# Performance work log

Hardware: AMD Instinct MI355X
Metric: run time of the kernel (lower is better)

The kernel has to match this reference:

```python
import jax, jax.numpy as jnp
import numpy as np
import math

B, LQ, LK = 4, 2048, 2048
DQ = DK = DV = ND = 512
H = 8
DS = ND // H
EPS = 1e-5


def _ln(x, g, b):
    m = jnp.mean(x, axis=-1, keepdims=True)
    v = jnp.mean((x - m) ** 2, axis=-1, keepdims=True)
    return (x - m) / jnp.sqrt(v + EPS) * g + b


def setup_inputs() -> dict:
    key = jax.random.key(0)
    ks = jax.random.split(key, 12)
    s = 0.02
    return {
        "Q": jax.random.normal(ks[0], (B, LQ, DQ), dtype=jnp.float32),
        "K": jax.random.normal(ks[1], (B, LK, DK), dtype=jnp.float32),
        "mask": jax.random.randint(ks[2], (B, LQ, LK), 0, 2, dtype=jnp.int32),
        "temperature": jax.random.uniform(ks[3], (B, LK, 1), dtype=jnp.float32, minval=0.5, maxval=1.5),
        "Wq": jax.random.normal(ks[4], (DQ, ND), dtype=jnp.float32) * s,
        "bq": jnp.zeros((ND,), dtype=jnp.float32),
        "Wk": jax.random.normal(ks[5], (DK, ND), dtype=jnp.float32) * s,
        "bk": jnp.zeros((ND,), dtype=jnp.float32),
        "Wv": jax.random.normal(ks[6], (DK, ND), dtype=jnp.float32) * s,
        "bv": jnp.zeros((ND,), dtype=jnp.float32),
        "Wo": jax.random.normal(ks[7], (ND, ND), dtype=jnp.float32) * s,
        "bo": jnp.zeros((ND,), dtype=jnp.float32),
        "ln0_g": jnp.ones((ND,), dtype=jnp.float32),
        "ln0_b": jnp.zeros((ND,), dtype=jnp.float32),
        "ln1_g": jnp.ones((ND,), dtype=jnp.float32),
        "ln1_b": jnp.zeros((ND,), dtype=jnp.float32),
    }


def reference(Q, K, mask, temperature, Wq, bq, Wk, bk, Wv, bv, Wo, bo, ln0_g, ln0_b, ln1_g, ln1_b):
    q = Q @ Wq + bq                                  # (B, Lq, ND)
    k = K @ Wk + bk                                  # (B, Lk, ND)
    v = K @ Wv + bv                                  # (B, Lk, ND)
    # torch's cat(split(ds,2),0) == head-major reshape; head h -> channels [h*ds:(h+1)*ds]
    qh = q.reshape(B, LQ, H, DS)
    kh = k.reshape(B, LK, H, DS)
    vh = v.reshape(B, LK, H, DS)
    A = jnp.einsum("bqhd,bkhd->bhqk", qh, kh) / math.sqrt(ND)
    # per-key temperature, broadcast over heads and queries
    A = A / temperature[:, None, :, 0][:, :, None, :]      # (B,H,Lq,Lk)
    A = jnp.where(mask[:, None, :, :] == 0, jnp.float32(-1e9), A)
    A = jax.nn.softmax(A, axis=-1)
    Oh = qh + jnp.einsum("bhqk,bkhd->bqhd", A, vh)          # residual with projected Q
    O = Oh.reshape(B, LQ, ND)
    O = _ln(O, ln0_g, ln0_b)
    O = O + jax.nn.relu(O @ Wo + bo)
    O = _ln(O, ln1_g, ln1_b)
    return O
```

## Files before the change

kernel.cpp:

```cpp
#include <hip/hip_runtime.h>

typedef __attribute__((ext_vector_type(8))) short bf16x8;
typedef __attribute__((ext_vector_type(16))) float f32x16;

#define MFMA32 __builtin_amdgcn_mfma_f32_32x32x16_bf16

__device__ __forceinline__ unsigned short bf16r(float f){
  unsigned u = __builtin_bit_cast(unsigned, f);
  unsigned r = (u + 0x7FFFu + ((u >> 16) & 1u)) >> 16;
  return (unsigned short)r;
}
__device__ __forceinline__ unsigned bfpack2(float a, float b){
  unsigned ua = __builtin_bit_cast(unsigned, a);
  unsigned ub = __builtin_bit_cast(unsigned, b);
  unsigned ra = (ua + 0x7FFFu + ((ua >> 16) & 1u)) >> 16;
  unsigned rb = (ub + 0x7FFFu + ((ub >> 16) & 1u)) & 0xFFFF0000u;
  return (ra & 0xFFFFu) | rb;
}
__device__ __forceinline__ float bf2f(unsigned short h){
  unsigned u = ((unsigned)h) << 16;
  return __builtin_bit_cast(float, u);
}
__device__ __forceinline__ unsigned cvtpk_bf16(float a, float b){
  unsigned r;
  asm("v_cvt_pk_bf16_f32 %0, %1, %2" : "=v"(r) : "v"(a), "v"(b));
  return r;
}
__device__ __forceinline__ void permswap(unsigned &x, unsigned &y){
  asm volatile("v_permlane32_swap_b32 %0, %1" : "+v"(x), "+v"(y));
}
__device__ __forceinline__ float fexp2(float x){
  float r; asm("v_exp_f32 %0, %1" : "=v"(r) : "v"(x)); return r;
}

__global__ __launch_bounds__(256) void wt_kernel(
    const float* __restrict__ W0, const float* __restrict__ W1,
    const float* __restrict__ W2, const float* __restrict__ W3,
    unsigned short* __restrict__ T0, unsigned short* __restrict__ T1,
    unsigned short* __restrict__ T2, unsigned short* __restrict__ T3)
{
  int z = blockIdx.z;
  const float* W = z==0?W0 : z==1?W1 : z==2?W2 : W3;
  unsigned short* T = z==0?T0 : z==1?T1 : z==2?T2 : T3;
  __shared__ float tile[64][68];
  int kb0 = blockIdx.x*64, nb0 = blockIdx.y*64;
  int tid = threadIdx.x;
#pragma unroll
  for (int i=0;i<4;++i){
    int c = tid + i*256; int r = c>>4, cc = (c&15)*4;
    *(float4*)&tile[r][cc] = *(const float4*)&W[(kb0+r)*512 + nb0 + cc];
  }
  __syncthreads();
#pragma unroll
  for (int i=0;i<4;++i){
    int c = tid + i*256; int o = c*4; int n = o>>6, kk = o&63;
    ushort4 pk;
    pk.x = bf16r(tile[kk+0][n]); pk.y = bf16r(tile[kk+1][n]);
    pk.z = bf16r(tile[kk+2][n]); pk.w = bf16r(tile[kk+3][n]);
    *(ushort4*)&T[(nb0+n)*512 + kb0 + kk] = pk;
  }
}

__global__ __launch_bounds__(256,2) void qkv_kernel(
    const float* __restrict__ Qin, const float* __restrict__ Kin,
    const unsigned short* __restrict__ WqT, const unsigned short* __restrict__ WkT,
    const unsigned short* __restrict__ WvT,
    const float* __restrict__ bq, const float* __restrict__ bk,
    const float* __restrict__ bv, const float* __restrict__ temp,
    unsigned short* __restrict__ qbuf, unsigned short* __restrict__ kbuf,
    unsigned short* __restrict__ vt)
{
  const float RS2K = 0.044194173824159216f * 1.4426950408889634f;
  __shared__ short SM[128*144];
  short (*As)[72] = (short(*)[72])SM;
  short (*Bs)[72] = (short(*)[72])(SM + 128*72);
  int z = blockIdx.z;
  const float* A = (z==0) ? Qin : Kin;
  const unsigned short* BT = z==0 ? WqT : (z==1 ? WkT : WvT);
  const float* bias = z==0 ? bq : (z==1 ? bk : bv);
  int m0 = blockIdx.x*128, n0 = blockIdx.y*128;
  int tid = threadIdx.x;
  int lane = tid & 63, w = tid >> 6, l5 = lane & 31, hi = lane >> 5;
  int wr = w >> 1, wc = w & 1;
  f32x16 acc00, acc01, acc10, acc11;
#pragma unroll
  for (int i=0;i<16;++i){ acc00[i]=0.f; acc01[i]=0.f; acc10[i]=0.f; acc11[i]=0.f; }

  for (int kt=0; kt<8; ++kt){
    int k0 = kt*64;
    __syncthreads();
#pragma unroll
    for (int i=0;i<4;++i){
      int c = tid + i*256; int r = c>>3, cc = (c&7)*8;
      const float* src = &A[(m0+r)*512 + k0 + cc];
      float4 v0 = *(const float4*)src;
      float4 v1 = *(const float4*)(src+4);
      uint4 pk;
      pk.x = bfpack2(v0.x, v0.y); pk.y = bfpack2(v0.z, v0.w);
      pk.z = bfpack2(v1.x, v1.y); pk.w = bfpack2(v1.z, v1.w);
      *(uint4*)&As[r][cc] = pk;
    }
#pragma unroll
    for (int i=0;i<4;++i){
      int c = tid + i*256; int r = c>>3, cc = (c&7)*8;
      *(uint4*)&Bs[r][cc] = *(const uint4*)&BT[(n0+r)*512 + k0 + cc];
    }
    __syncthreads();
#pragma unroll
    for (int ks=0; ks<4; ++ks){
      bf16x8 a0 = *(const bf16x8*)&As[wr*64 + l5     ][ks*16 + hi*8];
      bf16x8 a1 = *(const bf16x8*)&As[wr*64 + 32 + l5][ks*16 + hi*8];
      bf16x8 b0 = *(const bf16x8*)&Bs[wc*64 + l5     ][ks*16 + hi*8];
      bf16x8 b1 = *(const bf16x8*)&Bs[wc*64 + 32 + l5][ks*16 + hi*8];
      acc00 = MFMA32(a0, b0, acc00, 0,0,0);
      acc01 = MFMA32(a0, b1, acc01, 0,0,0);
      acc10 = MFMA32(a1, b0, acc10, 0,0,0);
      acc11 = MFMA32(a1, b1, acc11, 0,0,0);
    }
  }

  if (z <= 1){
    unsigned short* Cout = (z==0) ? qbuf : kbuf;
#pragma unroll
    for (int mt=0; mt<2; ++mt){
      float sc[16];
      if (z==1){
        int mb = m0 + wr*64 + mt*32 + 4*hi;
#pragma unroll
        for (int qd=0; qd<4; ++qd)
#pragma unroll
        for (int j=0; j<4; ++j)
          sc[qd*4+j] = RS2K*__builtin_amdgcn_rcpf(temp[mb + qd*8 + j]);
      }
#pragma unroll
      for (int nt=0; nt<2; ++nt){
        const f32x16& acc = mt==0 ? (nt==0?acc00:acc01) : (nt==0?acc10:acc11);
        int n = n0 + wc*64 + nt*32 + l5;
        float bn = bias[n];
#pragma unroll
        for (int r=0;r<16;++r){
          int m = m0 + wr*64 + mt*32 + (r&3) + 8*(r>>2) + 4*hi;
          float v = acc[r] + bn;
          if (z==1) v *= sc[r];
          Cout[m*512 + n] = bf16r(v);
        }
      }
    }
  } else {
    __syncthreads();
    short* Lt = SM;
#pragma unroll
    for (int mt=0; mt<2; ++mt)
#pragma unroll
    for (int nt=0; nt<2; ++nt){
      const f32x16& acc = mt==0 ? (nt==0?acc00:acc01) : (nt==0?acc10:acc11);
      int n = wc*64 + nt*32 + l5;
      float bn = bias[n0 + n];
#pragma unroll
      for (int qd=0; qd<4; ++qd){
        int mloc = wr*64 + mt*32 + qd*8 + 4*hi;
        uint2 pk;
        pk.x = bfpack2(acc[qd*4+0]+bn, acc[qd*4+1]+bn);
        pk.y = bfpack2(acc[qd*4+2]+bn, acc[qd*4+3]+bn);
        *(uint2*)&Lt[n*144 + mloc] = pk;
      }
    }
    __syncthreads();
    int b = m0 >> 11;
    int ktb = (m0 & 2047) >> 5;
#pragma unroll
    for (int pass=0; pass<2; ++pass){
      int d = (tid>>2) + pass*64;
      int kk0 = (tid&3)*8;
#pragma unroll
      for (int kt=0; kt<4; ++kt){
        uint4 v = *(const uint4*)&Lt[d*144 + kt*32 + kk0];
        *(uint4*)&vt[(size_t)((b*64 + ktb + kt)*512 + n0 + d)*32 + kk0] = v;
      }
    }
  }
}

__global__ __launch_bounds__(256,2) void gemm_o_kernel(
    const unsigned short* __restrict__ A, const unsigned short* __restrict__ BT,
    const float* __restrict__ bias, float* __restrict__ Cout,
    const unsigned short* __restrict__ resid)
{
  __shared__ short As[128][72];
  __shared__ short Bs[128][72];
  int m0 = blockIdx.x*128, n0 = blockIdx.y*128;
  int tid = threadIdx.x;
  int lane = tid & 63, w = tid >> 6, l5 = lane & 31, hi = lane >> 5;
  int wr = w >> 1, wc = w & 1;
  f32x16 acc00, acc01, acc10, acc11;
#pragma unroll
  for (int i=0;i<16;++i){ acc00[i]=0.f; acc01[i]=0.f; acc10[i]=0.f; acc11[i]=0.f; }

  for (int kt=0; kt<8; ++kt){
    int k0 = kt*64;
    __syncthreads();
#pragma unroll
    for (int i=0;i<4;++i){
      int c = tid + i*256; int r = c>>3, cc = (c&7)*8;
      *(uint4*)&As[r][cc] = *(const uint4*)&A[(m0+r)*512 + k0 + cc];
    }
#pragma unroll
    for (int i=0;i<4;++i){
      int c = tid + i*256; int r = c>>3, cc = (c&7)*8;
      *(uint4*)&Bs[r][cc] = *(const uint4*)&BT[(n0+r)*512 + k0 + cc];
    }
    __syncthreads();
#pragma unroll
    for (int ks=0; ks<4; ++ks){
      bf16x8 a0 = *(const bf16x8*)&As[wr*64 + l5     ][ks*16 + hi*8];
      bf16x8 a1 = *(const bf16x8*)&As[wr*64 + 32 + l5][ks*16 + hi*8];
      bf16x8 b0 = *(const bf16x8*)&Bs[wc*64 + l5     ][ks*16 + hi*8];
      bf16x8 b1 = *(const bf16x8*)&Bs[wc*64 + 32 + l5][ks*16 + hi*8];
      acc00 = MFMA32(a0, b0, acc00, 0,0,0);
      acc01 = MFMA32(a0, b1, acc01, 0,0,0);
      acc10 = MFMA32(a1, b0, acc10, 0,0,0);
      acc11 = MFMA32(a1, b1, acc11, 0,0,0);
    }
  }
#pragma unroll
  for (int mt=0; mt<2; ++mt){
#pragma unroll
    for (int nt=0; nt<2; ++nt){
      const f32x16& acc = mt==0 ? (nt==0?acc00:acc01) : (nt==0?acc10:acc11);
      int n = n0 + wc*64 + nt*32 + l5;
      float bn = bias[n];
#pragma unroll
      for (int r=0;r<16;++r){
        int m = m0 + wr*64 + mt*32 + (r&3) + 8*(r>>2) + 4*hi;
        float v = acc[r] + bn;
        Cout[m*512 + n] = fmaxf(v, 0.f) + bf2f(resid[m*512 + n]);
      }
    }
  }
}

__global__ __launch_bounds__(256,3) void attn_kernel(
    const unsigned short* __restrict__ qb, const unsigned short* __restrict__ kb,
    const unsigned short* __restrict__ vt, const int* __restrict__ mask,
    unsigned short* __restrict__ Op, float* __restrict__ lbuf)
{
  int bid = blockIdx.x;
  int swz = (bid & 7)*128 + (bid >> 3);
  int s  = swz & 1;
  int hv = (swz >> 1) & 1;
  int qt = (swz >> 2) & 63;
  int b  = swz >> 8;
  int q0 = qt * 32;

  __shared__ short Ks[32][264];
  __shared__ short Vs[256][40];
  __shared__ float BiasF[64*20];

  int tid = threadIdx.x;
  int lane = tid & 63, w = tid >> 6, l5 = lane & 31, hi = lane >> 5;

  bf16x8 qf0, qf1, qf2, qf3;
  {
    const unsigned short* qp = qb + (size_t)(b*2048 + q0 + l5)*512 + (hv*4 + w)*64 + hi*8;
    qf0 = *(const bf16x8*)(qp);
    qf1 = *(const bf16x8*)(qp + 16);
    qf2 = *(const bf16x8*)(qp + 32);
    qf3 = *(const bf16x8*)(qp + 48);
  }

  f32x16 o0, o1;
#pragma unroll
  for (int i=0;i<16;++i){ o0[i]=0.f; o1[i]=0.f; }
  float lsum = 0.f;

  const int kbeg = s*32, kend = s*32 + 32;
  const int kr0 = tid >> 5, kjc = (tid & 31)*8;
  const int vr0 = tid >> 2, vjc = (tid & 3)*8;
  const int qq = tid >> 3, kk4 = tid & 7;
  const unsigned short* kpb = kb + (size_t)(b*2048 + kr0)*512 + hv*256 + kjc;
  const unsigned short* vpb = vt + ((size_t)(b*64)*512 + hv*256)*32 + tid*8;
  const int* mpb = mask + (size_t)(b*2048 + q0 + qq)*2048 + kk4*4;

  uint4 rK0, rK1, rK2, rK3, rV0, rV1, rV2, rV3; int4 rM;
  {
    const unsigned short* kp = kpb + (size_t)kbeg*32*512;
    rK0 = *(const uint4*)(kp);
    rK1 = *(const uint4*)(kp + 8*512);
    rK2 = *(const uint4*)(kp + 16*512);
    rK3 = *(const uint4*)(kp + 24*512);
    const unsigned short* vp = vpb + (size_t)kbeg*512*32;
    rV0 = *(const uint4*)(vp);
    rV1 = *(const uint4*)(vp + 256*8);
    rV2 = *(const uint4*)(vp + 512*8);
    rV3 = *(const uint4*)(vp + 768*8);
    rM  = *(const int4*)(mpb + kbeg*32);
  }

  for (int kt=kbeg; kt<kend; ++kt){
    __syncthreads();
    *(uint4*)&Ks[kr0     ][kjc] = rK0;
    *(uint4*)&Ks[kr0 +  8][kjc] = rK1;
    *(uint4*)&Ks[kr0 + 16][kjc] = rK2;
    *(uint4*)&Ks[kr0 + 24][kjc] = rK3;
    *(uint4*)&Vs[vr0      ][vjc] = rV0;
    *(uint4*)&Vs[vr0 +  64][vjc] = rV1;
    *(uint4*)&Vs[vr0 + 128][vjc] = rV2;
    *(uint4*)&Vs[vr0 + 192][vjc] = rV3;
    {
      float4 bw;
      bw.x = rM.x ? 0.f : -1.44269504e9f;
      bw.y = rM.y ? 0.f : -1.44269504e9f;
      bw.z = rM.z ? 0.f : -1.44269504e9f;
      bw.w = rM.w ? 0.f : -1.44269504e9f;
      *(float4*)&BiasF[(qq + (kk4&1)*32)*20 + ((kk4>>1)<<2)] = bw;
    }
    if (kt+1 < kend){
      const unsigned short* kp = kpb + (size_t)(kt+1)*32*512;
      rK0 = *(const uint4*)(kp);
      rK1 = *(const uint4*)(kp + 8*512);
      rK2 = *(const uint4*)(kp + 16*512);
      rK3 = *(const uint4*)(kp + 24*512);
      const unsigned short* vp = vpb + (size_t)(kt+1)*512*32;
      rV0 = *(const uint4*)(vp);
      rV1 = *(const uint4*)(vp + 256*8);
      rV2 = *(const uint4*)(vp + 512*8);
      rV3 = *(const uint4*)(vp + 768*8);
      rM  = *(const int4*)(mpb + (kt+1)*32);
    }
    __syncthreads();

    f32x16 sA;
#pragma unroll
    for (int i=0;i<16;++i) sA[i] = 0.f;
    __builtin_amdgcn_s_setprio(1);
    {
      bf16x8 kf;
      kf = *(const bf16x8*)&Ks[l5][w*64 +  0 + hi*8]; sA = MFMA32(kf, qf0, sA, 0,0,0);
      kf = *(const bf16x8*)&Ks[l5][w*64 + 16 + hi*8]; sA = MFMA32(kf, qf1, sA, 0,0,0);
      kf = *(const bf16x8*)&Ks[l5][w*64 + 32 + hi*8]; sA = MFMA32(kf, qf2, sA, 0,0,0);
      kf = *(const bf16x8*)&Ks[l5][w*64 + 48 + hi*8]; sA = MFMA32(kf, qf3, sA, 0,0,0);
    }
    __builtin_amdgcn_s_setprio(0);

    float p0,p1,p2,p3,p4,p5,p6,p7,p8,p9,pa,pb,pc,pd,pe,pf;
    {
      float4 bq0 = *(const float4*)&BiasF[lane*20 + 0];
      p0 = fexp2(sA[0] + bq0.x);
      p1 = fexp2(sA[1] + bq0.y);
      p2 = fexp2(sA[2] + bq0.z);
      p3 = fexp2(sA[3] + bq0.w);
      float4 bq1 = *(const float4*)&BiasF[lane*20 + 4];
      p4 = fexp2(sA[4] + bq1.x);
      p5 = fexp2(sA[5] + bq1.y);
      p6 = fexp2(sA[6] + bq1.z);
      p7 = fexp2(sA[7] + bq1.w);
      float4 bq2 = *(const float4*)&BiasF[lane*20 + 8];
      p8 = fexp2(sA[8]  + bq2.x);
      p9 = fexp2(sA[9]  + bq2.y);
      pa = fexp2(sA[10] + bq2.z);
      pb = fexp2(sA[11] + bq2.w);
      float4 bq3 = *(const float4*)&BiasF[lane*20 + 12];
      pc = fexp2(sA[12] + bq3.x);
      pd = fexp2(sA[13] + bq3.y);
      pe = fexp2(sA[14] + bq3.z);
      pf = fexp2(sA[15] + bq3.w);
    }
    lsum += (((p0+p1)+(p2+p3)) + ((p4+p5)+(p6+p7))) +
            (((p8+p9)+(pa+pb)) + ((pc+pd)+(pe+pf)));

    unsigned a0w0 = cvtpk_bf16(p0, p1);
    unsigned a0w1 = cvtpk_bf16(p2, p3);
    unsigned a0w2 = cvtpk_bf16(p4, p5);
    unsigned a0w3 = cvtpk_bf16(p6, p7);
    permswap(a0w0, a0w2);
    permswap(a0w1, a0w3);
    unsigned a1w0 = cvtpk_bf16(p8, p9);
    unsigned a1w1 = cvtpk_bf16(pa, pb);
    unsigned a1w2 = cvtpk_bf16(pc, pd);
    unsigned a1w3 = cvtpk_bf16(pe, pf);
    permswap(a1w0, a1w2);
    permswap(a1w1, a1w3);
    uint4 u0; u0.x = a0w0; u0.y = a0w1; u0.z = a0w2; u0.w = a0w3;
    uint4 u1; u1.x = a1w0; u1.y = a1w1; u1.z = a1w2; u1.w = a1w3;
    bf16x8 pa0 = __builtin_bit_cast(bf16x8, u0);
    bf16x8 pa1 = __builtin_bit_cast(bf16x8, u1);

    bf16x8 v00 = *(const bf16x8*)&Vs[w*64      + l5][hi*8];
    bf16x8 v01 = *(const bf16x8*)&Vs[w*64      + l5][16 + hi*8];
    bf16x8 v10 = *(const bf16x8*)&Vs[w*64 + 32 + l5][hi*8];
    bf16x8 v11 = *(const bf16x8*)&Vs[w*64 + 32 + l5][16 + hi*8];
    __builtin_amdgcn_s_setprio(1);
    o0 = MFMA32(pa0, v00, o0, 0,0,0);
    o0 = MFMA32(pa1, v01, o0, 0,0,0);
    o1 = MFMA32(pa0, v10, o1, 0,0,0);
    o1 = MFMA32(pa1, v11, o1, 0,0,0);
    __builtin_amdgcn_s_setprio(0);
  }

  float lfull = lsum + __shfl_xor(lsum, 32, 64);
  if (hi == 0){
    lbuf[(size_t)(b*2048 + q0 + l5)*16 + s*8 + (hv*4 + w)] = lfull;
  }
  unsigned short* op = Op + (size_t)s * 4194304u;
#pragma unroll
  for (int nt=0; nt<2; ++nt){
#pragma unroll
    for (int r=0;r<16;++r){
      int qlocal = (r&3) + 8*(r>>2) + 4*hi;
      int q = q0 + qlocal;
      int d = hv*256 + w*64 + nt*32 + l5;
      op[(size_t)(b*2048 + q)*512 + d] = bf16r(nt==0 ? o0[r] : o1[r]);
    }
  }
}

__global__ __launch_bounds__(256) void combine_ln_kernel(
    const unsigned short* __restrict__ OpA, const unsigned short* __restrict__ OpB,
    const float* __restrict__ lbuf, const unsigned short* __restrict__ qb,
    const float* __restrict__ g, const float* __restrict__ be,
    unsigned short* __restrict__ Y)
{
  int row = blockIdx.x*4 + (threadIdx.x >> 6);
  int lane = threadIdx.x & 63;
  int h = lane >> 3;
  float lA = lbuf[(size_t)row*16 + h];
  float lB = lbuf[(size_t)row*16 + 8 + h];
  float inv = __builtin_amdgcn_rcpf(lA + lB);
  size_t base = (size_t)row*512 + lane*8;
  bf16x8 a  = *(const bf16x8*)&OpA[base];
  bf16x8 bb = *(const bf16x8*)&OpB[base];
  bf16x8 qv = *(const bf16x8*)&qb[base];
  float x0 = (bf2f((unsigned short)a[0]) + bf2f((unsigned short)bb[0]))*inv + bf2f((unsigned short)qv[0]);
  float x1 = (bf2f((unsigned short)a[1]) + bf2f((unsigned short)bb[1]))*inv + bf2f((unsigned short)qv[1]);
  float x2 = (bf2f((unsigned short)a[2]) + bf2f((unsigned short)bb[2]))*inv + bf2f((unsigned short)qv[2]);
  float x3 = (bf2f((unsigned short)a[3]) + bf2f((unsigned short)bb[3]))*inv + bf2f((unsigned short)qv[3]);
  float x4 = (bf2f((unsigned short)a[4]) + bf2f((unsigned short)bb[4]))*inv + bf2f((unsigned short)qv[4]);
  float x5 = (bf2f((unsigned short)a[5]) + bf2f((unsigned short)bb[5]))*inv + bf2f((unsigned short)qv[5]);
  float x6 = (bf2f((unsigned short)a[6]) + bf2f((unsigned short)bb[6]))*inv + bf2f((unsigned short)qv[6]);
  float x7 = (bf2f((unsigned short)a[7]) + bf2f((unsigned short)bb[7]))*inv + bf2f((unsigned short)qv[7]);
  float sm = ((x0+x1)+(x2+x3)) + ((x4+x5)+(x6+x7));
#pragma unroll
  for (int m=1; m<64; m<<=1) sm += __shfl_xor(sm, m, 64);
  float mean = sm * (1.0f/512.0f);
  float d0=x0-mean, d1=x1-mean, d2=x2-mean, d3=x3-mean;
  float d4=x4-mean, d5=x5-mean, d6=x6-mean, d7=x7-mean;
  float s2 = ((d0*d0+d1*d1)+(d2*d2+d3*d3)) + ((d4*d4+d5*d5)+(d6*d6+d7*d7));
#pragma unroll
  for (int m=1; m<64; m<<=1) s2 += __shfl_xor(s2, m, 64);
  float rstd = rsqrtf(s2*(1.0f/512.0f) + 1e-5f);
  const float* gp = g + lane*8; const float* bp = be + lane*8;
  float4 g0 = *(const float4*)gp, g1 = *(const float4*)(gp+4);
  float4 b0 = *(const float4*)bp, b1 = *(const float4*)(bp+4);
  uint4 yo;
  yo.x = bfpack2(d0*rstd*g0.x + b0.x, d1*rstd*g0.y + b0.y);
  yo.y = bfpack2(d2*rstd*g0.z + b0.z, d3*rstd*g0.w + b0.w);
  yo.z = bfpack2(d4*rstd*g1.x + b1.x, d5*rstd*g1.y + b1.y);
  yo.w = bfpack2(d6*rstd*g1.z + b1.z, d7*rstd*g1.w + b1.w);
  *(uint4*)&Y[base] = yo;
}

__global__ __launch_bounds__(256) void ln_kernel(
    const float* __restrict__ X, const float* __restrict__ g,
    const float* __restrict__ be, float* __restrict__ Y)
{
  int row = blockIdx.x*4 + (threadIdx.x >> 6);
  int lane = threadIdx.x & 63;
  const float* x = X + (size_t)row*512 + lane*8;
  float4 v0 = *(const float4*)x;
  float4 v1 = *(const float4*)(x + 4);
  float s = ((v0.x+v0.y)+(v0.z+v0.w)) + ((v1.x+v1.y)+(v1.z+v1.w));
#pragma unroll
  for (int m=1; m<64; m<<=1) s += __shfl_xor(s, m, 64);
  float mean = s * (1.0f/512.0f);
  float d0=v0.x-mean, d1=v0.y-mean, d2=v0.z-mean, d3=v0.w-mean;
  float d4=v1.x-mean, d5=v1.y-mean, d6=v1.z-mean, d7=v1.w-mean;
  float s2 = ((d0*d0+d1*d1)+(d2*d2+d3*d3)) + ((d4*d4+d5*d5)+(d6*d6+d7*d7));
#pragma unroll
  for (int m=1; m<64; m<<=1) s2 += __shfl_xor(s2, m, 64);
  float rstd = rsqrtf(s2*(1.0f/512.0f) + 1e-5f);
  const float* gp = g + lane*8; const float* bp = be + lane*8;
  float4 g0 = *(const float4*)gp, g1 = *(const float4*)(gp+4);
  float4 b0 = *(const float4*)bp, b1 = *(const float4*)(bp+4);
  float4 y0, y1;
  y0.x = d0*rstd*g0.x + b0.x; y0.y = d1*rstd*g0.y + b0.y;
  y0.z = d2*rstd*g0.z + b0.z; y0.w = d3*rstd*g0.w + b0.w;
  y1.x = d4*rstd*g1.x + b1.x; y1.y = d5*rstd*g1.y + b1.y;
  y1.z = d6*rstd*g1.z + b1.z; y1.w = d7*rstd*g1.w + b1.w;
  float* yp = Y + (size_t)row*512 + lane*8;
  *(float4*)yp = y0;
  *(float4*)(yp+4) = y1;
}

extern "C" void kernel_launch(void* const* d_in, const int* in_sizes, int n_in,
                              void* d_out, int out_size, void* d_ws, size_t ws_size,
                              hipStream_t stream) {
  const float* Q    = (const float*)d_in[0];
  const float* K    = (const float*)d_in[1];
  const int*   mask = (const int*)d_in[2];
  const float* temp = (const float*)d_in[3];
  const float* Wq = (const float*)d_in[4];  const float* bq = (const float*)d_in[5];
  const float* Wk = (const float*)d_in[6];  const float* bk = (const float*)d_in[7];
  const float* Wv = (const float*)d_in[8];  const float* bv = (const float*)d_in[9];
  const float* Wo = (const float*)d_in[10]; const float* bo = (const float*)d_in[11];
  const float* g0 = (const float*)d_in[12]; const float* b0 = (const float*)d_in[13];
  const float* g1 = (const float*)d_in[14]; const float* b1 = (const float*)d_in[15];
  float* out = (float*)d_out;
  (void)in_sizes; (void)n_in; (void)out_size; (void)ws_size;

  char* ws = (char*)d_ws;
  unsigned short* qbuf = (unsigned short*)(ws + 0);
  unsigned short* kbuf = (unsigned short*)(ws + 8388608);
  unsigned short* vtb  = (unsigned short*)(ws + 16777216);
  unsigned short* OpA  = (unsigned short*)(ws + 25165824);
  unsigned short* WqT  = (unsigned short*)(ws + 41943040);
  unsigned short* WkT  = WqT + 262144;
  unsigned short* WvT  = WqT + 524288;
  unsigned short* WoT  = WqT + 786432;
  float* lbuf = (float*)(ws + 44040192);
  unsigned short* Olnf = (unsigned short*)(ws + 8388608);
  float* O2   = (float*)(ws + 25165824);

  wt_kernel<<<dim3(8,8,4), 256, 0, stream>>>(Wq, Wk, Wv, Wo, WqT, WkT, WvT, WoT);
  qkv_kernel<<<dim3(64,4,3), 256, 0, stream>>>(Q, K, WqT, WkT, WvT, bq, bk, bv, temp,
                                               qbuf, kbuf, vtb);
  attn_kernel<<<1024, 256, 0, stream>>>(qbuf, kbuf, vtb, mask, OpA, lbuf);
  combine_ln_kernel<<<2048, 256, 0, stream>>>(OpA, OpA + 4194304, lbuf, qbuf, g0, b0, Olnf);
  gemm_o_kernel<<<dim3(64,4), 256, 0, stream>>>(Olnf, WoT, bo, O2, Olnf);
  ln_kernel<<<2048, 256, 0, stream>>>(O2, g1, b1, out);
}
```

Baseline: 145.6 us.

## Drop LDS staging in attention, load K/V/mask directly to registers, double query tile

The attention kernel no longer stages K, V and the mask bias through shared memory with two barriers per iteration. Each wave now loads its own K/V fragments and mask words straight into registers and software-prefetches the next tile. Each block handles 64 queries (two 32-row halves) so every K/V fragment is reused twice, and the grid is halved. The cost is more VGPRs (launch bounds drop to two blocks per CU) and uncoalesced per-lane mask loads. There is also less parallelism across the grid.

```diff
diff --git a/kernel.cpp b/kernel.cpp
--- a/kernel.cpp
+++ b/kernel.cpp
@@ -239,167 +239,192 @@
   }
 }
 
-__global__ __launch_bounds__(256,3) void attn_kernel(
+__global__ __launch_bounds__(256,2) void attn_kernel(
     const unsigned short* __restrict__ qb, const unsigned short* __restrict__ kb,
     const unsigned short* __restrict__ vt, const int* __restrict__ mask,
     unsigned short* __restrict__ Op, float* __restrict__ lbuf)
 {
   int bid = blockIdx.x;
-  int swz = (bid & 7)*128 + (bid >> 3);
-  int s  = swz & 1;
-  int hv = (swz >> 1) & 1;
-  int qt = (swz >> 2) & 63;
-  int b  = swz >> 8;
-  int q0 = qt * 32;
-
-  __shared__ short Ks[32][264];
-  __shared__ short Vs[256][40];
-  __shared__ float BiasF[64*20];
+  int swz = (bid & 7)*64 + (bid >> 3);
+  int hv = swz & 1;
+  int qt = (swz >> 1) & 31;
+  int g  = swz >> 6;
+  int b  = g >> 1, s = g & 1;
+  int q0 = qt * 64;
 
   int tid = threadIdx.x;
   int lane = tid & 63, w = tid >> 6, l5 = lane & 31, hi = lane >> 5;
-
-  bf16x8 qf0, qf1, qf2, qf3;
+  int hcho = hv*256 + w*64;
+
+  bf16x8 qlo0,qlo1,qlo2,qlo3, qhi0,qhi1,qhi2,qhi3;
   {
-    const unsigned short* qp = qb + (size_t)(b*2048 + q0 + l5)*512 + (hv*4 + w)*64 + hi*8;
-    qf0 = *(const bf16x8*)(qp);
-    qf1 = *(const bf16x8*)(qp + 16);
-    qf2 = *(const bf16x8*)(qp + 32);
-    qf3 = *(const bf16x8*)(qp + 48);
-  }
-
-  f32x16 o0, o1;
-#pragma unroll
-  for (int i=0;i<16;++i){ o0[i]=0.f; o1[i]=0.f; }
-  float lsum = 0.f;
+    const unsigned short* qp = qb + (size_t)(b*2048 + q0 + l5)*512 + hcho + hi*8;
+    qlo0 = *(const bf16x8*)(qp);
+    qlo1 = *(const bf16x8*)(qp + 16);
+    qlo2 = *(const bf16x8*)(qp + 32);
+    qlo3 = *(const bf16x8*)(qp + 48);
+    qp += (size_t)32*512;
+    qhi0 = *(const bf16x8*)(qp);
+    qhi1 = *(const bf16x8*)(qp + 16);
+    qhi2 = *(const bf16x8*)(qp + 32);
+    qhi3 = *(const bf16x8*)(qp + 48);
+  }
+
+  f32x16 oL0, oL1, oH0, oH1;
+#pragma unroll
+  for (int i=0;i<16;++i){ oL0[i]=0.f; oL1[i]=0.f; oH0[i]=0.f; oH1[i]=0.f; }
+  float lsumL = 0.f, lsumH = 0.f;
 
   const int kbeg = s*32, kend = s*32 + 32;
-  const int kr0 = tid >> 5, kjc = (tid & 31)*8;
-  const int vr0 = tid >> 2, vjc = (tid & 3)*8;
-  const int qq = tid >> 3, kk4 = tid & 7;
-  const unsigned short* kpb = kb + (size_t)(b*2048 + kr0)*512 + hv*256 + kjc;
-  const unsigned short* vpb = vt + ((size_t)(b*64)*512 + hv*256)*32 + tid*8;
-  const int* mpb = mask + (size_t)(b*2048 + q0 + qq)*2048 + kk4*4;
-
-  uint4 rK0, rK1, rK2, rK3, rV0, rV1, rV2, rV3; int4 rM;
+  const unsigned short* kp0 = kb + (size_t)(b*2048 + l5)*512 + hcho + hi*8;
+  const unsigned short* vp0 = vt + ((size_t)(b*64)*512 + hcho + l5)*32 + hi*8;
+  const int* mpl0 = mask + (size_t)(b*2048 + q0 + l5)*2048 + 4*hi;
+  const int* mph0 = mpl0 + (size_t)32*2048;
+
+  uint4 kA,kB,kC,kD, vA,vB,vC,vD;
+  int4 mL0,mL1,mL2,mL3, mH0,mH1,mH2,mH3;
   {
-    const unsigned short* kp = kpb + (size_t)kbeg*32*512;
-    rK0 = *(const uint4*)(kp);
-    rK1 = *(const uint4*)(kp + 8*512);
-    rK2 = *(const uint4*)(kp + 16*512);
-    rK3 = *(const uint4*)(kp + 24*512);
-    const unsigned short* vp = vpb + (size_t)kbeg*512*32;
-    rV0 = *(const uint4*)(vp);
-    rV1 = *(const uint4*)(vp + 256*8);
-    rV2 = *(const uint4*)(vp + 512*8);
-    rV3 = *(const uint4*)(vp + 768*8);
-    rM  = *(const int4*)(mpb + kbeg*32);
+    const unsigned short* kp = kp0 + (size_t)kbeg*32*512;
+    kA = *(const uint4*)(kp);      kB = *(const uint4*)(kp + 16);
+    kC = *(const uint4*)(kp + 32); kD = *(const uint4*)(kp + 48);
+    const unsigned short* vp = vp0 + (size_t)kbeg*512*32;
+    vA = *(const uint4*)(vp);        vB = *(const uint4*)(vp + 16);
+    vC = *(const uint4*)(vp + 1024); vD = *(const uint4*)(vp + 1040);
+    const int* ml = mpl0 + kbeg*32;
+    mL0 = *(const int4*)(ml);      mL1 = *(const int4*)(ml + 8);
+    mL2 = *(const int4*)(ml + 16); mL3 = *(const int4*)(ml + 24);
+    const int* mh = mph0 + kbeg*32;
+    mH0 = *(const int4*)(mh);      mH1 = *(const int4*)(mh + 8);
+    mH2 = *(const int4*)(mh + 16); mH3 = *(const int4*)(mh + 24);
   }
 
   for (int kt=kbeg; kt<kend; ++kt){
-    __syncthreads();
-    *(uint4*)&Ks[kr0     ][kjc] = rK0;
-    *(uint4*)&Ks[kr0 +  8][kjc] = rK1;
-    *(uint4*)&Ks[kr0 + 16][kjc] = rK2;
-    *(uint4*)&Ks[kr0 + 24][kjc] = rK3;
-    *(uint4*)&Vs[vr0      ][vjc] = rV0;
-    *(uint4*)&Vs[vr0 +  64][vjc] = rV1;
-    *(uint4*)&Vs[vr0 + 128][vjc] = rV2;
-    *(uint4*)&Vs[vr0 + 192][vjc] = rV3;
-    {
-      float4 bw;
-      bw.x = rM.x ? 0.f : -1.44269504e9f;
-      bw.y = rM.y ? 0.f : -1.44269504e9f;
-      bw.z = rM.z ? 0.f : -1.44269504e9f;
-      bw.w = rM.w ? 0.f : -1.44269504e9f;
-      *(float4*)&BiasF[(qq + (kk4&1)*32)*20 + ((kk4>>1)<<2)] = bw;
-    }
-    if (kt+1 < kend){
-      const unsigned short* kp = kpb + (size_t)(kt+1)*32*512;
-      rK0 = *(const uint4*)(kp);
-      rK1 = *(const uint4*)(kp + 8*512);
-      rK2 = *(const uint4*)(kp + 16*512);
-      rK3 = *(const uint4*)(kp + 24*512);
-      const unsigned short* vp = vpb + (size_t)(kt+1)*512*32;
-      rV0 = *(const uint4*)(vp);
-      rV1 = *(const uint4*)(vp + 256*8);
-      rV2 = *(const uint4*)(vp + 512*8);
-      rV3 = *(const uint4*)(vp + 768*8);
-      rM  = *(const int4*)(mpb + (kt+1)*32);
-    }
-    __syncthreads();
-
+    bool more = (kt+1 < kend);
     f32x16 sA;
 #pragma unroll
     for (int i=0;i<16;++i) sA[i] = 0.f;
     __builtin_amdgcn_s_setprio(1);
-    {
-      bf16x8 kf;
-      kf = *(const bf16x8*)&Ks[l5][w*64 +  0 + hi*8]; sA = MFMA32(kf, qf0, sA, 0,0,0);
-      kf = *(const bf16x8*)&Ks[l5][w*64 + 16 + hi*8]; sA = MFMA32(kf, qf1, sA, 0,0,0);
-      kf = *(const bf16x8*)&Ks[l5][w*64 + 32 + hi*8]; sA = MFMA32(kf, qf2, sA, 0,0,0);
-      kf = *(const bf16x8*)&Ks[l5][w*64 + 48 + hi*8]; sA = MFMA32(kf, qf3, sA, 0,0,0);
-    }
+    sA = MFMA32(__builtin_bit_cast(bf16x8,kA), qlo0, sA, 0,0,0);
+    sA = MFMA32(__builtin_bit_cast(bf16x8,kB), qlo1, sA, 0,0,0);
+    sA = MFMA32(__builtin_bit_cast(bf16x8,kC), qlo2, sA, 0,0,0);
+    sA = MFMA32(__builtin_bit_cast(bf16x8,kD), qlo3, sA, 0,0,0);
     __builtin_amdgcn_s_setprio(0);
-
     float p0,p1,p2,p3,p4,p5,p6,p7,p8,p9,pa,pb,pc,pd,pe,pf;
-    {
-      float4 bq0 = *(const float4*)&BiasF[lane*20 + 0];
-      p0 = fexp2(sA[0] + bq0.x);
-      p1 = fexp2(sA[1] + bq0.y);
-      p2 = fexp2(sA[2] + bq0.z);
-      p3 = fexp2(sA[3] + bq0.w);
-      float4 bq1 = *(const float4*)&BiasF[lane*20 + 4];
-      p4 = fexp2(sA[4] + bq1.x);
-      p5 = fexp2(sA[5] + bq1.y);
-      p6 = fexp2(sA[6] + bq1.z);
-      p7 = fexp2(sA[7] + bq1.w);
-      float4 bq2 = *(const float4*)&BiasF[lane*20 + 8];
-      p8 = fexp2(sA[8]  + bq2.x);
-      p9 = fexp2(sA[9]  + bq2.y);
-      pa = fexp2(sA[10] + bq2.z);
-      pb = fexp2(sA[11] + bq2.w);
-      float4 bq3 = *(const float4*)&BiasF[lane*20 + 12];
-      pc = fexp2(sA[12] + bq3.x);
-      pd = fexp2(sA[13] + bq3.y);
-      pe = fexp2(sA[14] + bq3.z);
-      pf = fexp2(sA[15] + bq3.w);
-    }
-    lsum += (((p0+p1)+(p2+p3)) + ((p4+p5)+(p6+p7))) +
-            (((p8+p9)+(pa+pb)) + ((pc+pd)+(pe+pf)));
-
-    unsigned a0w0 = cvtpk_bf16(p0, p1);
-    unsigned a0w1 = cvtpk_bf16(p2, p3);
-    unsigned a0w2 = cvtpk_bf16(p4, p5);
-    unsigned a0w3 = cvtpk_bf16(p6, p7);
-    permswap(a0w0, a0w2);
-    permswap(a0w1, a0w3);
-    unsigned a1w0 = cvtpk_bf16(p8, p9);
-    unsigned a1w1 = cvtpk_bf16(pa, pb);
-    unsigned a1w2 = cvtpk_bf16(pc, pd);
-    unsigned a1w3 = cvtpk_bf16(pe, pf);
-    permswap(a1w0, a1w2);
-    permswap(a1w1, a1w3);
-    uint4 u0; u0.x = a0w0; u0.y = a0w1; u0.z = a0w2; u0.w = a0w3;
-    uint4 u1; u1.x = a1w0; u1.y = a1w1; u1.z = a1w2; u1.w = a1w3;
-    bf16x8 pa0 = __builtin_bit_cast(bf16x8, u0);
-    bf16x8 pa1 = __builtin_bit_cast(bf16x8, u1);
-
-    bf16x8 v00 = *(const bf16x8*)&Vs[w*64      + l5][hi*8];
-    bf16x8 v01 = *(const bf16x8*)&Vs[w*64      + l5][16 + hi*8];
-    bf16x8 v10 = *(const bf16x8*)&Vs[w*64 + 32 + l5][hi*8];
-    bf16x8 v11 = *(const bf16x8*)&Vs[w*64 + 32 + l5][16 + hi*8];
+    p0 = fexp2(mL0.x ? sA[0]  : -1.44269504e9f);
+    p1 = fexp2(mL0.y ? sA[1]  : -1.44269504e9f);
+    p2 = fexp2(mL0.z ? sA[2]  : -1.44269504e9f);
+    p3 = fexp2(mL0.w ? sA[3]  : -1.44269504e9f);
+    p4 = fexp2(mL1.x ? sA[4]  : -1.44269504e9f);
+    p5 = fexp2(mL1.y ? sA[5]  : -1.44269504e9f);
+    p6 = fexp2(mL1.z ? sA[6]  : -1.44269504e9f);
+    p7 = fexp2(mL1.w ? sA[7]  : -1.44269504e9f);
+    p8 = fexp2(mL2.x ? sA[8]  : -1.44269504e9f);
+    p9 = fexp2(mL2.y ? sA[9]  : -1.44269504e9f);
+    pa = fexp2(mL2.z ? sA[10] : -1.44269504e9f);
+    pb = fexp2(mL2.w ? sA[11] : -1.44269504e9f);
+    pc = fexp2(mL3.x ? sA[12] : -1.44269504e9f);
+    pd = fexp2(mL3.y ? sA[13] : -1.44269504e9f);
+    pe = fexp2(mL3.z ? sA[14] : -1.44269504e9f);
+    pf = fexp2(mL3.w ? sA[15] : -1.44269504e9f);
+    lsumL += (((p0+p1)+(p2+p3)) + ((p4+p5)+(p6+p7))) +
+             (((p8+p9)+(pa+pb)) + ((pc+pd)+(pe+pf)));
+    if (more){
+      const int* ml = mpl0 + (kt+1)*32;
+      mL0 = *(const int4*)(ml);      mL1 = *(const int4*)(ml + 8);
+      mL2 = *(const int4*)(ml + 16); mL3 = *(const int4*)(ml + 24);
+    }
+    unsigned uL0 = cvtpk_bf16(p0, p1);
+    unsigned uL1 = cvtpk_bf16(p2, p3);
+    unsigned uL2 = cvtpk_bf16(p4, p5);
+    unsigned uL3 = cvtpk_bf16(p6, p7);
+    permswap(uL0, uL2); permswap(uL1, uL3);
+    unsigned uL4 = cvtpk_bf16(p8, p9);
+    unsigned uL5 = cvtpk_bf16(pa, pb);
+    unsigned uL6 = cvtpk_bf16(pc, pd);
+    unsigned uL7 = cvtpk_bf16(pe, pf);
+    permswap(uL4, uL6); permswap(uL5, uL7);
+    uint4 w0; w0.x=uL0; w0.y=uL1; w0.z=uL2; w0.w=uL3;
+    uint4 w1; w1.x=uL4; w1.y=uL5; w1.z=uL6; w1.w=uL7;
+    bf16x8 paL0 = __builtin_bit_cast(bf16x8, w0);
+    bf16x8 paL1 = __builtin_bit_cast(bf16x8, w1);
+
+#pragma unroll
+    for (int i=0;i<16;++i) sA[i] = 0.f;
     __builtin_amdgcn_s_setprio(1);
-    o0 = MFMA32(pa0, v00, o0, 0,0,0);
-    o0 = MFMA32(pa1, v01, o0, 0,0,0);
-    o1 = MFMA32(pa0, v10, o1, 0,0,0);
-    o1 = MFMA32(pa1, v11, o1, 0,0,0);
+    sA = MFMA32(__builtin_bit_cast(bf16x8,kA), qhi0, sA, 0,0,0);
+    sA = MFMA32(__builtin_bit_cast(bf16x8,kB), qhi1, sA, 0,0,0);
+    sA = MFMA32(__builtin_bit_cast(bf16x8,kC), qhi2, sA, 0,0,0);
+    sA = MFMA32(__builtin_bit_cast(bf16x8,kD), qhi3, sA, 0,0,0);
     __builtin_amdgcn_s_setprio(0);
-  }
-
-  float lfull = lsum + __shfl_xor(lsum, 32, 64);
+    if (more){
+      const unsigned short* kp = kp0 + (size_t)(kt+1)*32*512;
+      kA = *(const uint4*)(kp);      kB = *(const uint4*)(kp + 16);
+      kC = *(const uint4*)(kp + 32); kD = *(const uint4*)(kp + 48);
+    }
+    p0 = fexp2(mH0.x ? sA[0]  : -1.44269504e9f);
+    p1 = fexp2(mH0.y ? sA[1]  : -1.44269504e9f);
+    p2 = fexp2(mH0.z ? sA[2]  : -1.44269504e9f);
+    p3 = fexp2(mH0.w ? sA[3]  : -1.44269504e9f);
+    p4 = fexp2(mH1.x ? sA[4]  : -1.44269504e9f);
+    p5 = fexp2(mH1.y ? sA[5]  : -1.44269504e9f);
+    p6 = fexp2(mH1.z ? sA[6]  : -1.44269504e9f);
+    p7 = fexp2(mH1.w ? sA[7]  : -1.44269504e9f);
+    p8 = fexp2(mH2.x ? sA[8]  : -1.44269504e9f);
+    p9 = fexp2(mH2.y ? sA[9]  : -1.44269504e9f);
+    pa = fexp2(mH2.z ? sA[10] : -1.44269504e9f);
+    pb = fexp2(mH2.w ? sA[11] : -1.44269504e9f);
+    pc = fexp2(mH3.x ? sA[12] : -1.44269504e9f);
+    pd = fexp2(mH3.y ? sA[13] : -1.44269504e9f);
+    pe = fexp2(mH3.z ? sA[14] : -1.44269504e9f);
+    pf = fexp2(mH3.w ? sA[15] : -1.44269504e9f);
+    lsumH += (((p0+p1)+(p2+p3)) + ((p4+p5)+(p6+p7))) +
+             (((p8+p9)+(pa+pb)) + ((pc+pd)+(pe+pf)));
+    if (more){
+      const int* mh = mph0 + (kt+1)*32;
+      mH0 = *(const int4*)(mh);      mH1 = *(const int4*)(mh + 8);
+      mH2 = *(const int4*)(mh + 16); mH3 = *(const int4*)(mh + 24);
+    }
+    unsigned uH0 = cvtpk_bf16(p0, p1);
+    unsigned uH1 = cvtpk_bf16(p2, p3);
+    unsigned uH2 = cvtpk_bf16(p4, p5);
+    unsigned uH3 = cvtpk_bf16(p6, p7);
+    permswap(uH0, uH2); permswap(uH1, uH3);
+    unsigned uH4 = cvtpk_bf16(p8, p9);
+    unsigned uH5 = cvtpk_bf16(pa, pb);
+    unsigned uH6 = cvtpk_bf16(pc, pd);
+    unsigned uH7 = cvtpk_bf16(pe, pf);
+    permswap(uH4, uH6); permswap(uH5, uH7);
+    uint4 w2; w2.x=uH0; w2.y=uH1; w2.z=uH2; w2.w=uH3;
+    uint4 w3; w3.x=uH4; w3.y=uH5; w3.z=uH6; w3.w=uH7;
+    bf16x8 paH0 = __builtin_bit_cast(bf16x8, w2);
+    bf16x8 paH1 = __builtin_bit_cast(bf16x8, w3);
+
+    bf16x8 v00 = __builtin_bit_cast(bf16x8, vA);
+    bf16x8 v01 = __builtin_bit_cast(bf16x8, vB);
+    bf16x8 v10 = __builtin_bit_cast(bf16x8, vC);
+    bf16x8 v11 = __builtin_bit_cast(bf16x8, vD);
+    __builtin_amdgcn_s_setprio(1);
+    oL0 = MFMA32(paL0, v00, oL0, 0,0,0);
+    oL0 = MFMA32(paL1, v01, oL0, 0,0,0);
+    oL1 = MFMA32(paL0, v10, oL1, 0,0,0);
+    oL1 = MFMA32(paL1, v11, oL1, 0,0,0);
+    oH0 = MFMA32(paH0, v00, oH0, 0,0,0);
+    oH0 = MFMA32(paH1, v01, oH0, 0,0,0);
+    oH1 = MFMA32(paH0, v10, oH1, 0,0,0);
+    oH1 = MFMA32(paH1, v11, oH1, 0,0,0);
+    __builtin_amdgcn_s_setprio(0);
+    if (more){
+      const unsigned short* vp = vp0 + (size_t)(kt+1)*512*32;
+      vA = *(const uint4*)(vp);        vB = *(const uint4*)(vp + 16);
+      vC = *(const uint4*)(vp + 1024); vD = *(const uint4*)(vp + 1040);
+    }
+  }
+
+  float lfullL = lsumL + __shfl_xor(lsumL, 32, 64);
+  float lfullH = lsumH + __shfl_xor(lsumH, 32, 64);
   if (hi == 0){
-    lbuf[(size_t)(b*2048 + q0 + l5)*16 + s*8 + (hv*4 + w)] = lfull;
+    lbuf[(size_t)(b*2048 + q0 + l5)*16      + s*8 + (hv*4 + w)] = lfullL;
+    lbuf[(size_t)(b*2048 + q0 + 32 + l5)*16 + s*8 + (hv*4 + w)] = lfullH;
   }
   unsigned short* op = Op + (size_t)s * 4194304u;
 #pragma unroll
@@ -407,9 +432,9 @@
 #pragma unroll
     for (int r=0;r<16;++r){
       int qlocal = (r&3) + 8*(r>>2) + 4*hi;
-      int q = q0 + qlocal;
-      int d = hv*256 + w*64 + nt*32 + l5;
-      op[(size_t)(b*2048 + q)*512 + d] = bf16r(nt==0 ? o0[r] : o1[r]);
+      int d = hcho + nt*32 + l5;
+      op[(size_t)(b*2048 + q0 + qlocal)*512 + d]      = bf16r(nt==0 ? oL0[r] : oL1[r]);
+      op[(size_t)(b*2048 + q0 + 32 + qlocal)*512 + d] = bf16r(nt==0 ? oH0[r] : oH1[r]);
     }
   }
 }
@@ -523,7 +548,7 @@
   wt_kernel<<<dim3(8,8,4), 256, 0, stream>>>(Wq, Wk, Wv, Wo, WqT, WkT, WvT, WoT);
   qkv_kernel<<<dim3(64,4,3), 256, 0, stream>>>(Q, K, WqT, WkT, WvT, bq, bk, bv, temp,
                                                qbuf, kbuf, vtb);
-  attn_kernel<<<1024, 256, 0, stream>>>(qbuf, kbuf, vtb, mask, OpA, lbuf);
+  attn_kernel<<<512, 256, 0, stream>>>(qbuf, kbuf, vtb, mask, OpA, lbuf);
   combine_ln_kernel<<<2048, 256, 0, stream>>>(OpA, OpA + 4194304, lbuf, qbuf, g0, b0, Olnf);
   gemm_o_kernel<<<dim3(64,4), 256, 0, stream>>>(Olnf, WoT, bo, O2, Olnf);
   ln_kernel<<<2048, 256, 0, stream>>>(O2, g1, b1, out);
```

Measured after the change: 177.0 us. +21.6%, slower.

## Bit-pack mask in a prepass and load K/V fragments directly into registers

Applied to the files above, without the earlier changes.

Adds a kernel that compresses the int32 mask into one bit per key using wave ballots, laid out so each attention lane reads one 32-bit word per key tile. The attention kernel drops its shared-memory staging of K, V and the mask bias. Each wave now loads its MFMA operand fragments straight from global memory into registers and prefetches the next tile, which removes both per-tile __syncthreads barriers. Occupancy is raised from 3 to 4 blocks per CU. In exchange there is an extra kernel launch that reads the full mask, and the four waves no longer share K/V through LDS, so each fetches its own slices from global memory or cache.

```diff
diff --git a/kernel.cpp b/kernel.cpp
--- a/kernel.cpp
+++ b/kernel.cpp
@@ -58,6 +58,25 @@
     pk.x = bf16r(tile[kk+0][n]); pk.y = bf16r(tile[kk+1][n]);
     pk.z = bf16r(tile[kk+2][n]); pk.w = bf16r(tile[kk+3][n]);
     *(ushort4*)&T[(nb0+n)*512 + kb0 + kk] = pk;
+  }
+}
+
+__global__ __launch_bounds__(256) void maskc_kernel(
+    const int* __restrict__ mask, unsigned* __restrict__ bm)
+{
+  int tid = threadIdx.x; int lane = tid & 63; int w = tid >> 6;
+  int gw = blockIdx.x*4 + w;
+  int b = gw >> 11, q = gw & 2047;
+  const int* mp = mask + ((size_t)(b*2048 + q))*2048 + lane;
+  unsigned* bp = bm + (size_t)(b*64)*2048 + q;
+#pragma unroll 4
+  for (int g=0; g<32; ++g){
+    int v = mp[g*64];
+    unsigned long long bal = __ballot(v != 0);
+    if (lane == 0){
+      bp[(size_t)(g*2    )*2048] = (unsigned)bal;
+      bp[(size_t)(g*2 + 1)*2048] = (unsigned)(bal >> 32);
+    }
   }
 }
 
@@ -239,11 +258,12 @@
   }
 }
 
-__global__ __launch_bounds__(256,3) void attn_kernel(
+__global__ __launch_bounds__(256,4) void attn_kernel(
     const unsigned short* __restrict__ qb, const unsigned short* __restrict__ kb,
-    const unsigned short* __restrict__ vt, const int* __restrict__ mask,
+    const unsigned short* __restrict__ vt, const unsigned* __restrict__ bm,
     unsigned short* __restrict__ Op, float* __restrict__ lbuf)
 {
+  const float NEG = -1.44269504e9f;
   int bid = blockIdx.x;
   int swz = (bid & 7)*128 + (bid >> 3);
   int s  = swz & 1;
@@ -252,16 +272,13 @@
   int b  = swz >> 8;
   int q0 = qt * 32;
 
-  __shared__ short Ks[32][264];
-  __shared__ short Vs[256][40];
-  __shared__ float BiasF[64*20];
-
   int tid = threadIdx.x;
   int lane = tid & 63, w = tid >> 6, l5 = lane & 31, hi = lane >> 5;
+  int hcho = hv*256 + w*64;
 
   bf16x8 qf0, qf1, qf2, qf3;
   {
-    const unsigned short* qp = qb + (size_t)(b*2048 + q0 + l5)*512 + (hv*4 + w)*64 + hi*8;
+    const unsigned short* qp = qb + (size_t)(b*2048 + q0 + l5)*512 + hcho + hi*8;
     qf0 = *(const bf16x8*)(qp);
     qf1 = *(const bf16x8*)(qp + 16);
     qf2 = *(const bf16x8*)(qp + 32);
@@ -274,127 +291,92 @@
   float lsum = 0.f;
 
   const int kbeg = s*32, kend = s*32 + 32;
-  const int kr0 = tid >> 5, kjc = (tid & 31)*8;
-  const int vr0 = tid >> 2, vjc = (tid & 3)*8;
-  const int qq = tid >> 3, kk4 = tid & 7;
-  const unsigned short* kpb = kb + (size_t)(b*2048 + kr0)*512 + hv*256 + kjc;
-  const unsigned short* vpb = vt + ((size_t)(b*64)*512 + hv*256)*32 + tid*8;
-  const int* mpb = mask + (size_t)(b*2048 + q0 + qq)*2048 + kk4*4;
-
-  uint4 rK0, rK1, rK2, rK3, rV0, rV1, rV2, rV3; int4 rM;
+  const unsigned short* kp0 = kb + (size_t)(b*2048 + l5)*512 + hcho + hi*8;
+  const unsigned short* vp0 = vt + ((size_t)(b*64)*512 + hcho + l5)*32 + hi*8;
+  const unsigned* bp0 = bm + (size_t)(b*64)*2048 + q0 + l5;
+
+  uint4 kA,kB,kC,kD, vA,vB,vC,vD; unsigned bmw;
   {
-    const unsigned short* kp = kpb + (size_t)kbeg*32*512;
-    rK0 = *(const uint4*)(kp);
-    rK1 = *(const uint4*)(kp + 8*512);
-    rK2 = *(const uint4*)(kp + 16*512);
-    rK3 = *(const uint4*)(kp + 24*512);
-    const unsigned short* vp = vpb + (size_t)kbeg*512*32;
-    rV0 = *(const uint4*)(vp);
-    rV1 = *(const uint4*)(vp + 256*8);
-    rV2 = *(const uint4*)(vp + 512*8);
-    rV3 = *(const uint4*)(vp + 768*8);
-    rM  = *(const int4*)(mpb + kbeg*32);
+    const unsigned short* kp = kp0 + (size_t)kbeg*32*512;
+    kA = *(const uint4*)(kp);      kB = *(const uint4*)(kp + 16);
+    kC = *(const uint4*)(kp + 32); kD = *(const uint4*)(kp + 48);
+    const unsigned short* vp = vp0 + (size_t)kbeg*512*32;
+    vA = *(const uint4*)(vp);        vB = *(const uint4*)(vp + 16);
+    vC = *(const uint4*)(vp + 1024); vD = *(const uint4*)(vp + 1040);
+    bmw = bp0[(size_t)kbeg*2048];
   }
 
   for (int kt=kbeg; kt<kend; ++kt){
-    __syncthreads();
-    *(uint4*)&Ks[kr0     ][kjc] = rK0;
-    *(uint4*)&Ks[kr0 +  8][kjc] = rK1;
-    *(uint4*)&Ks[kr0 + 16][kjc] = rK2;
-    *(uint4*)&Ks[kr0 + 24][kjc] = rK3;
-    *(uint4*)&Vs[vr0      ][vjc] = rV0;
-    *(uint4*)&Vs[vr0 +  64][vjc] = rV1;
-    *(uint4*)&Vs[vr0 + 128][vjc] = rV2;
-    *(uint4*)&Vs[vr0 + 192][vjc] = rV3;
-    {
-      float4 bw;
-      bw.x = rM.x ? 0.f : -1.44269504e9f;
-      bw.y = rM.y ? 0.f : -1.44269504e9f;
-      bw.z = rM.z ? 0.f : -1.44269504e9f;
-      bw.w = rM.w ? 0.f : -1.44269504e9f;
-      *(float4*)&BiasF[(qq + (kk4&1)*32)*20 + ((kk4>>1)<<2)] = bw;
-    }
-    if (kt+1 < kend){
-      const unsigned short* kp = kpb + (size_t)(kt+1)*32*512;
-      rK0 = *(const uint4*)(kp);
-      rK1 = *(const uint4*)(kp + 8*512);
-      rK2 = *(const uint4*)(kp + 16*512);
-      rK3 = *(const uint4*)(kp + 24*512);
-      const unsigned short* vp = vpb + (size_t)(kt+1)*512*32;
-      rV0 = *(const uint4*)(vp);
-      rV1 = *(const uint4*)(vp + 256*8);
-      rV2 = *(const uint4*)(vp + 512*8);
-      rV3 = *(const uint4*)(vp + 768*8);
-      rM  = *(const int4*)(mpb + (kt+1)*32);
-    }
-    __syncthreads();
-
+    bool more = (kt+1 < kend);
     f32x16 sA;
 #pragma unroll
     for (int i=0;i<16;++i) sA[i] = 0.f;
     __builtin_amdgcn_s_setprio(1);
-    {
-      bf16x8 kf;
-      kf = *(const bf16x8*)&Ks[l5][w*64 +  0 + hi*8]; sA = MFMA32(kf, qf0, sA, 0,0,0);
-      kf = *(const bf16x8*)&Ks[l5][w*64 + 16 + hi*8]; sA = MFMA32(kf, qf1, sA, 0,0,0);
-      kf = *(const bf16x8*)&Ks[l5][w*64 + 32 + hi*8]; sA = MFMA32(kf, qf2, sA, 0,0,0);
-      kf = *(const bf16x8*)&Ks[l5][w*64 + 48 + hi*8]; sA = MFMA32(kf, qf3, sA, 0,0,0);
-    }
+    sA = MFMA32(__builtin_bit_cast(bf16x8,kA), qf0, sA, 0,0,0);
+    sA = MFMA32(__builtin_bit_cast(bf16x8,kB), qf1, sA, 0,0,0);
+    sA = MFMA32(__builtin_bit_cast(bf16x8,kC), qf2, sA, 0,0,0);
+    sA = MFMA32(__builtin_bit_cast(bf16x8,kD), qf3, sA, 0,0,0);
     __builtin_amdgcn_s_setprio(0);
-
+    if (more){
+      const unsigned short* kp = kp0 + (size_t)(kt+1)*32*512;
+      kA = *(const uint4*)(kp);      kB = *(const uint4*)(kp + 16);
+      kC = *(const uint4*)(kp + 32); kD = *(const uint4*)(kp + 48);
+    }
+    unsigned n0 = bmw >> (4*hi);
+    unsigned n1 = bmw >> (8 + 4*hi);
+    unsigned n2 = bmw >> (16 + 4*hi);
+    unsigned n3 = bmw >> (24 + 4*hi);
+    if (more) bmw = bp0[(size_t)(kt+1)*2048];
     float p0,p1,p2,p3,p4,p5,p6,p7,p8,p9,pa,pb,pc,pd,pe,pf;
-    {
-      float4 bq0 = *(const float4*)&BiasF[lane*20 + 0];
-      p0 = fexp2(sA[0] + bq0.x);
-      p1 = fexp2(sA[1] + bq0.y);
-      p2 = fexp2(sA[2] + bq0.z);
-      p3 = fexp2(sA[3] + bq0.w);
-      float4 bq1 = *(const float4*)&BiasF[lane*20 + 4];
-      p4 = fexp2(sA[4] + bq1.x);
-      p5 = fexp2(sA[5] + bq1.y);
-      p6 = fexp2(sA[6] + bq1.z);
-      p7 = fexp2(sA[7] + bq1.w);
-      float4 bq2 = *(const float4*)&BiasF[lane*20 + 8];
-      p8 = fexp2(sA[8]  + bq2.x);
-      p9 = fexp2(sA[9]  + bq2.y);
-      pa = fexp2(sA[10] + bq2.z);
-      pb = fexp2(sA[11] + bq2.w);
-      float4 bq3 = *(const float4*)&BiasF[lane*20 + 12];
-      pc = fexp2(sA[12] + bq3.x);
-      pd = fexp2(sA[13] + bq3.y);
-      pe = fexp2(sA[14] + bq3.z);
-      pf = fexp2(sA[15] + bq3.w);
-    }
+    p0 = fexp2((n0&1) ? sA[0]  : NEG);
+    p1 = fexp2((n0&2) ? sA[1]  : NEG);
+    p2 = fexp2((n0&4) ? sA[2]  : NEG);
+    p3 = fexp2((n0&8) ? sA[3]  : NEG);
+    p4 = fexp2((n1&1) ? sA[4]  : NEG);
+    p5 = fexp2((n1&2) ? sA[5]  : NEG);
+    p6 = fexp2((n1&4) ? sA[6]  : NEG);
+    p7 = fexp2((n1&8) ? sA[7]  : NEG);
+    p8 = fexp2((n2&1) ? sA[8]  : NEG);
+    p9 = fexp2((n2&2) ? sA[9]  : NEG);
+    pa = fexp2((n2&4) ? sA[10] : NEG);
+    pb = fexp2((n2&8) ? sA[11] : NEG);
+    pc = fexp2((n3&1) ? sA[12] : NEG);
+    pd = fexp2((n3&2) ? sA[13] : NEG);
+    pe = fexp2((n3&4) ? sA[14] : NEG);
+    pf = fexp2((n3&8) ? sA[15] : NEG);
     lsum += (((p0+p1)+(p2+p3)) + ((p4+p5)+(p6+p7))) +
             (((p8+p9)+(pa+pb)) + ((pc+pd)+(pe+pf)));
 
-    unsigned a0w0 = cvtpk_bf16(p0, p1);
-    unsigned a0w1 = cvtpk_bf16(p2, p3);
-    unsigned a0w2 = cvtpk_bf16(p4, p5);
-    unsigned a0w3 = cvtpk_bf16(p6, p7);
-    permswap(a0w0, a0w2);
-    permswap(a0w1, a0w3);
-    unsigned a1w0 = cvtpk_bf16(p8, p9);
-    unsigned a1w1 = cvtpk_bf16(pa, pb);
-    unsigned a1w2 = cvtpk_bf16(pc, pd);
-    unsigned a1w3 = cvtpk_bf16(pe, pf);
-    permswap(a1w0, a1w2);
-    permswap(a1w1, a1w3);
-    uint4 u0; u0.x = a0w0; u0.y = a0w1; u0.z = a0w2; u0.w = a0w3;
-    uint4 u1; u1.x = a1w0; u1.y = a1w1; u1.z = a1w2; u1.w = a1w3;
-    bf16x8 pa0 = __builtin_bit_cast(bf16x8, u0);
-    bf16x8 pa1 = __builtin_bit_cast(bf16x8, u1);
-
-    bf16x8 v00 = *(const bf16x8*)&Vs[w*64      + l5][hi*8];
-    bf16x8 v01 = *(const bf16x8*)&Vs[w*64      + l5][16 + hi*8];
-    bf16x8 v10 = *(const bf16x8*)&Vs[w*64 + 32 + l5][hi*8];
-    bf16x8 v11 = *(const bf16x8*)&Vs[w*64 + 32 + l5][16 + hi*8];
+    unsigned u0 = cvtpk_bf16(p0, p1);
+    unsigned u1 = cvtpk_bf16(p2, p3);
+    unsigned u2 = cvtpk_bf16(p4, p5);
+    unsigned u3 = cvtpk_bf16(p6, p7);
+    permswap(u0, u2); permswap(u1, u3);
+    unsigned u4 = cvtpk_bf16(p8, p9);
+    unsigned u5 = cvtpk_bf16(pa, pb);
+    unsigned u6 = cvtpk_bf16(pc, pd);
+    unsigned u7 = cvtpk_bf16(pe, pf);
+    permswap(u4, u6); permswap(u5, u7);
+    uint4 w0; w0.x=u0; w0.y=u1; w0.z=u2; w0.w=u3;
+    uint4 w1; w1.x=u4; w1.y=u5; w1.z=u6; w1.w=u7;
+    bf16x8 pa0 = __builtin_bit_cast(bf16x8, w0);
+    bf16x8 pa1 = __builtin_bit_cast(bf16x8, w1);
+
+    bf16x8 v00 = __builtin_bit_cast(bf16x8, vA);
+    bf16x8 v01 = __builtin_bit_cast(bf16x8, vB);
+    bf16x8 v10 = __builtin_bit_cast(bf16x8, vC);
+    bf16x8 v11 = __builtin_bit_cast(bf16x8, vD);
     __builtin_amdgcn_s_setprio(1);
     o0 = MFMA32(pa0, v00, o0, 0,0,0);
     o0 = MFMA32(pa1, v01, o0, 0,0,0);
     o1 = MFMA32(pa0, v10, o1, 0,0,0);
     o1 = MFMA32(pa1, v11, o1, 0,0,0);
     __builtin_amdgcn_s_setprio(0);
+    if (more){
+      const unsigned short* vp = vp0 + (size_t)(kt+1)*512*32;
+      vA = *(const uint4*)(vp);        vB = *(const uint4*)(vp + 16);
+      vC = *(const uint4*)(vp + 1024); vD = *(const uint4*)(vp + 1040);
+    }
   }
 
   float lfull = lsum + __shfl_xor(lsum, 32, 64);
@@ -407,9 +389,8 @@
 #pragma unroll
     for (int r=0;r<16;++r){
       int qlocal = (r&3) + 8*(r>>2) + 4*hi;
-      int q = q0 + qlocal;
-      int d = hv*256 + w*64 + nt*32 + l5;
-      op[(size_t)(b*2048 + q)*512 + d] = bf16r(nt==0 ? o0[r] : o1[r]);
+      int d = hcho + nt*32 + l5;
+      op[(size_t)(b*2048 + q0 + qlocal)*512 + d] = bf16r(nt==0 ? o0[r] : o1[r]);
     }
   }
 }
@@ -517,13 +498,15 @@
   unsigned short* WvT  = WqT + 524288;
   unsigned short* WoT  = WqT + 786432;
   float* lbuf = (float*)(ws + 44040192);
+  unsigned* bmb = (unsigned*)(ws + 44564480);
   unsigned short* Olnf = (unsigned short*)(ws + 8388608);
   float* O2   = (float*)(ws + 25165824);
 
   wt_kernel<<<dim3(8,8,4), 256, 0, stream>>>(Wq, Wk, Wv, Wo, WqT, WkT, WvT, WoT);
+  maskc_kernel<<<2048, 256, 0, stream>>>(mask, bmb);
   qkv_kernel<<<dim3(64,4,3), 256, 0, stream>>>(Q, K, WqT, WkT, WvT, bq, bk, bv, temp,
                                                qbuf, kbuf, vtb);
-  attn_kernel<<<1024, 256, 0, stream>>>(qbuf, kbuf, vtb, mask, OpA, lbuf);
+  attn_kernel<<<1024, 256, 0, stream>>>(qbuf, kbuf, vtb, bmb, OpA, lbuf);
   combine_ln_kernel<<<2048, 256, 0, stream>>>(OpA, OpA + 4194304, lbuf, qbuf, g0, b0, Olnf);
   gemm_o_kernel<<<dim3(64,4), 256, 0, stream>>>(Olnf, WoT, bo, O2, Olnf);
   ln_kernel<<<2048, 256, 0, stream>>>(O2, g1, b1, out);
```

Measured after the change: 178.5 us. +22.6%, slower.
